# Performance work log

Measured on AMD Instinct MI355X. Metric: run time of the kernel, lower is better.

The kernel has to match this reference:

```python
import jax, jax.numpy as jnp
import numpy as np

B, LQ, LKV = 2, 2048, 2048
C, CTX, H, DK = 1024, 768, 16, 64
SCALE = DK ** (-0.5)


def setup_inputs() -> dict:
    key = jax.random.key(0)
    kx, ky, kq, kkv, kp, kb = jax.random.split(key, 6)
    # weights stored as [in, out] so projection is x @ W
    return {
        "x": jax.random.normal(kx, (B, LQ, C), dtype=jnp.float32),
        "y": jax.random.normal(ky, (B, LKV, CTX), dtype=jnp.float32),
        "Wq": jax.random.normal(kq, (C, H * DK), dtype=jnp.float32) * (C ** -0.5),
        "Wkv": jax.random.normal(kkv, (CTX, 2 * H * DK), dtype=jnp.float32) * (CTX ** -0.5),
        "Wproj": jax.random.normal(kp, (H * DK, C), dtype=jnp.float32) * ((H * DK) ** -0.5),
        "bproj": jax.random.normal(kb, (C,), dtype=jnp.float32) * 0.01,
    }


def reference(x, y, Wq, Wkv, Wproj, bproj):
    b, lq, _ = x.shape
    lkv = y.shape[1]
    # Q projection: [b, lq, H*DK] -> [b, H, lq, DK]
    q = (x @ Wq).reshape(b, lq, H, DK).transpose(0, 2, 1, 3)
    kv = (y @ Wkv).reshape(b, lkv, 2, H, DK).transpose(2, 0, 3, 1, 4)
    k, v = kv[0], kv[1]
    # attention scores [b, H, lq, lkv], stable softmax, no dropout (Identity)
    atten = jax.nn.softmax(jnp.einsum("bhid,bhjd->bhij", q, k) * SCALE, axis=-1)
    res = jnp.einsum("bhij,bhjd->bhid", atten, v)  # [b, H, lq, DK]
    res = res.transpose(0, 2, 1, 3).reshape(b, lq, H * DK)
    out = res @ Wproj + bproj  # [b, lq, C]
    return out
```

## Files before the change

kernel.cpp:

```cpp
#include <hip/hip_runtime.h>
#include <hip/hip_bf16.h>
#include <cstdint>

typedef unsigned short u16;
typedef __attribute__((ext_vector_type(4))) float f32x4;
typedef __attribute__((ext_vector_type(8))) short s16x8;
typedef __attribute__((ext_vector_type(4))) unsigned int u32x4;

#define B_    2
#define LQ_   2048
#define LKV_  2048
#define H_    16
#define QSCALE_ 0.18033688011112042f

__device__ __forceinline__ u16 f2b(float f) {
  union { float f; unsigned int u; } v; v.f = f;
  unsigned int r = v.u + 0x7fffu + ((v.u >> 16) & 1u);
  return (u16)(r >> 16);
}

__device__ __forceinline__ unsigned cvtpk(float lo, float hi) {
  unsigned r;
  asm("v_cvt_pk_bf16_f32 %0, %1, %2" : "=v"(r) : "v"(lo), "v"(hi));
  return r;
}

#if __has_builtin(__builtin_amdgcn_exp2f)
__device__ __forceinline__ float fexp2(float x) { return __builtin_amdgcn_exp2f(x); }
#else
__device__ __forceinline__ float fexp2(float x) {
  float r; asm volatile("v_exp_f32 %0, %1" : "=v"(r) : "v"(x)); return r;
}
#endif

#define GLOAD(g, l) __builtin_amdgcn_global_load_lds( \
    (const __attribute__((address_space(1))) void*)(g), \
    (__attribute__((address_space(3))) void*)(l), 16, 0, 0)

__global__ void prep(const float* __restrict__ x, u16* __restrict__ xb,
                     const float* __restrict__ y, u16* __restrict__ yb,
                     const float* __restrict__ Wq, u16* __restrict__ WqT,
                     const float* __restrict__ Wkv, u16* __restrict__ WkvT,
                     const float* __restrict__ Wp, u16* __restrict__ WpT) {
  __shared__ u16 tile[64][65];
  const int bid = blockIdx.x;
  const int t = threadIdx.x;
  if (bid < 7168) {
    const float* in; u16* out; int i;
    if (bid < 4096) { in = x; out = xb; i = (bid * 256 + t) * 4; }
    else            { in = y; out = yb; i = ((bid - 4096) * 256 + t) * 4; }
    float4 v = *reinterpret_cast<const float4*>(in + i);
    ushort4 r;
    r.x = f2b(v.x); r.y = f2b(v.y); r.z = f2b(v.z); r.w = f2b(v.w);
    *reinterpret_cast<ushort4*>(out + i) = r;
    return;
  }
  const int tb = bid - 7168;
  const float* W; u16* WT; int K, N, bx, by;
  if (tb < 256)      { W = Wq;  WT = WqT;  K = 1024; N = 1024; bx = tb & 15;         by = tb >> 4; }
  else if (tb < 640) { W = Wkv; WT = WkvT; K = 768;  N = 2048; bx = (tb - 256) & 31; by = (tb - 256) >> 5; }
  else               { W = Wp;  WT = WpT;  K = 1024; N = 1024; bx = (tb - 640) & 15; by = (tb - 640) >> 4; }
  const int n0 = bx * 64, k0 = by * 64;
#pragma unroll
  for (int p = 0; p < 4; ++p) {
    int r = (t >> 4) + p * 16;
    int c = (t & 15) * 4;
    float4 v = *reinterpret_cast<const float4*>(W + (size_t)(k0 + r) * N + n0 + c);
    tile[r][c + 0] = f2b(v.x);
    tile[r][c + 1] = f2b(v.y);
    tile[r][c + 2] = f2b(v.z);
    tile[r][c + 3] = f2b(v.w);
  }
  __syncthreads();
#pragma unroll
  for (int p = 0; p < 4; ++p) {
    int nr = (t >> 4) + p * 16;
    int kc = (t & 15) * 4;
    ushort4 o;
    o.x = tile[kc + 0][nr];
    o.y = tile[kc + 1][nr];
    o.z = tile[kc + 2][nr];
    o.w = tile[kc + 3][nr];
    *reinterpret_cast<ushort4*>(WT + (size_t)(n0 + nr) * K + k0 + kc) = o;
  }
}

__device__ __forceinline__ void gemm_core(
    int OM, const u16* __restrict__ A, const u16* __restrict__ BT,
    u16* __restrict__ Cb, float* __restrict__ Cf,
    const float* __restrict__ bias, u16* __restrict__ VTp,
    int N, int K, int m0, int n0, char* smem) {
  const int tid = threadIdx.x;
  const int w = tid >> 6, lane = tid & 63;
  const int l16 = lane & 15, lk = lane >> 4;
  const int wm = w >> 1, wn = w & 1;
  const int NS = K >> 6;

  f32x4 acc[4][2];
#pragma unroll
  for (int i = 0; i < 4; ++i)
#pragma unroll
    for (int j = 0; j < 2; ++j)
      acc[i][j] = (f32x4){0.f, 0.f, 0.f, 0.f};

  const int srow = tid >> 3;
  const int sck = (tid & 7) ^ (srow & 7);
  const u16* gA = A + (size_t)(m0 + srow) * K + sck * 8;
  const u16* gB = BT + (size_t)(n0 + srow) * K + sck * 8;
  char* dA = smem + w * 1024;
  char* dB = smem + 32768 + w * 1024;

  auto stage = [&](int k0, int bb) {
#pragma unroll
    for (int i = 0; i < 4; ++i)
      GLOAD(gA + (size_t)i * 32 * K + k0, dA + bb * 16384 + i * 4096);
#pragma unroll
    for (int i = 0; i < 2; ++i)
      GLOAD(gB + (size_t)i * 32 * K + k0, dB + bb * 8192 + i * 4096);
  };

  const int swa = (l16 & 7) << 4;

  stage(0, 0);
  __syncthreads();
  int cur = 0;
  for (int s = 0; s < NS; ++s) {
    if (s + 1 < NS) stage((s + 1) * 64, cur ^ 1);
    const char* sAb = smem + cur * 16384;
    const char* sBb = smem + 32768 + cur * 8192;
#pragma unroll
    for (int kk = 0; kk < 2; ++kk) {
      s16x8 af[4], bf[2];
#pragma unroll
      for (int mt = 0; mt < 4; ++mt)
        af[mt] = *reinterpret_cast<const s16x8*>(
            sAb + (wm * 64 + mt * 16 + l16) * 128 + ((kk * 64 + lk * 16) ^ swa));
#pragma unroll
      for (int nt = 0; nt < 2; ++nt)
        bf[nt] = *reinterpret_cast<const s16x8*>(
            sBb + (wn * 32 + nt * 16 + l16) * 128 + ((kk * 64 + lk * 16) ^ swa));
      __builtin_amdgcn_s_setprio(1);
#pragma unroll
      for (int mt = 0; mt < 4; ++mt)
#pragma unroll
        for (int nt = 0; nt < 2; ++nt)
          acc[mt][nt] = __builtin_amdgcn_mfma_f32_16x16x32_bf16(af[mt], bf[nt], acc[mt][nt], 0, 0, 0);
      __builtin_amdgcn_s_setprio(0);
    }
    __syncthreads();
    cur ^= 1;
  }

#pragma unroll
  for (int mt = 0; mt < 4; ++mt) {
#pragma unroll
    for (int nt = 0; nt < 2; ++nt) {
      const int col = n0 + wn * 32 + nt * 16 + l16;
      const int row0 = m0 + wm * 64 + mt * 16 + lk * 4;
      if (OM == 2 && col >= 1024) {
        int b = row0 >> 11, kv = row0 & 2047;
        int h = (col >> 6) & 15, d = col & 63;
        ushort4 o;
        o.x = f2b(acc[mt][nt][0]); o.y = f2b(acc[mt][nt][1]);
        o.z = f2b(acc[mt][nt][2]); o.w = f2b(acc[mt][nt][3]);
        *reinterpret_cast<ushort4*>(VTp + (((size_t)(b * 16 + h) * 64 + d) * 2048 + kv)) = o;
      } else {
#pragma unroll
        for (int j = 0; j < 4; ++j) {
          int row = row0 + j;
          if (OM == 3)      Cb[(size_t)row * N + col] = f2b(acc[mt][nt][j] * QSCALE_);
          else if (OM == 2) Cb[(size_t)row * 1024 + col] = f2b(acc[mt][nt][j]);
          else              Cf[(size_t)row * N + col] = acc[mt][nt][j] + bias[col];
        }
      }
    }
  }
}

__global__ __launch_bounds__(256, 3)
void gemm_qkv(const u16* __restrict__ xb, const u16* __restrict__ WqT,
              const u16* __restrict__ yb, const u16* __restrict__ WkvT,
              u16* __restrict__ Qb, u16* __restrict__ Kbf, u16* __restrict__ VTb) {
  __shared__ __attribute__((aligned(16))) char smem[49152];
  const int bid = blockIdx.x;
  if (bid < 512) {
    gemm_core(3, xb, WqT, Qb, nullptr, nullptr, nullptr,
              1024, 1024, (bid & 31) * 128, (bid >> 5) * 64, smem);
  } else {
    const int t = bid - 512;
    gemm_core(2, yb, WkvT, Kbf, nullptr, nullptr, VTb,
              2048, 768, (t & 31) * 128, (t >> 5) * 64, smem);
  }
}

__global__ __launch_bounds__(256, 3)
void gemm_proj(const u16* __restrict__ Rb, const u16* __restrict__ WpT,
               float* __restrict__ out, const float* __restrict__ bias) {
  __shared__ __attribute__((aligned(16))) char smem[49152];
  const int bid = blockIdx.x;
  gemm_core(1, Rb, WpT, nullptr, out, bias, nullptr,
            1024, 1024, (bid & 31) * 128, (bid >> 5) * 64, smem);
}

__global__ __launch_bounds__(512, 4)
void flash_attn(const u16* __restrict__ Kq, const u16* __restrict__ Qb,
                const u16* __restrict__ VT, u16* __restrict__ Rb) {
  __shared__ __attribute__((aligned(16))) char smem[65536];
  __shared__ float dmerge[512 * 2];

  const int tid = threadIdx.x;
  const int w = tid >> 6, l = tid & 63;
  const int l16 = l & 15, lk = l >> 4;
  const int half = w >> 2, w4 = w & 3;

  const int bid = blockIdx.x;
  const int wg = ((bid & 7) << 6) | (bid >> 3);
  const int qt = wg & 15, bh = wg >> 4;
  const int b = bh >> 4, h = bh & 15;
  const int qrow0 = qt * 128 + w4 * 32;

  const u16* qp = Qb + ((size_t)(b * LQ_ + qrow0 + l16)) * 1024 + h * 64;
  s16x8 qf[2][2];
#pragma unroll
  for (int g = 0; g < 2; ++g)
#pragma unroll
    for (int ksq = 0; ksq < 2; ++ksq)
      qf[g][ksq] = *reinterpret_cast<const s16x8*>(qp + g * 16 * 1024 + ksq * 32 + lk * 8);

  f32x4 Oacc[2][4], Osum[2];
#pragma unroll
  for (int g = 0; g < 2; ++g) {
    Osum[g] = (f32x4){0.f, 0.f, 0.f, 0.f};
#pragma unroll
    for (int dt = 0; dt < 4; ++dt) Oacc[g][dt] = (f32x4){0.f, 0.f, 0.f, 0.f};
  }

  const u16* Kg = Kq + ((size_t)(b * LKV_ + half * 1024)) * 1024 + h * 64;
  const u16* Vg = VT + ((size_t)bh * 64) * 2048 + half * 1024;
  char* Kl = smem + half * 32768;
  char* Vl = smem + half * 32768 + 16384;

  s16x8 ones;
#pragma unroll
  for (int i = 0; i < 8; ++i) ones[i] = (short)0x3F80;

  const int r0 = ((l16 >> 2) << 3) + (l16 & 3);
  const int swk = ((l16 & 3) | (((l16 >> 2) & 1) << 2)) << 4;
  const int swv = (l16 & 7) << 4;

  const int srow = (tid & 255) >> 3;
  const int sck = (tid & 7) ^ ((srow & 3) | (((srow >> 3) & 1) << 2));
  const int scv = (tid & 7) ^ (srow & 7);
  const u16* kp0 = Kg + (size_t)srow * 1024 + sck * 8;
  const u16* kp1 = kp0 + (size_t)32 * 1024;
  const u16* vp0 = Vg + (size_t)srow * 2048 + scv * 8;
  const u16* vp1 = vp0 + (size_t)32 * 2048;
  char* kd0 = Kl + w4 * 1024;
  char* vd0 = Vl + w4 * 1024;

  auto stage = [&](int bb) {
    GLOAD(kp0, kd0 + bb * 8192);
    GLOAD(kp1, kd0 + bb * 8192 + 4096);
    GLOAD(vp0, vd0 + bb * 8192);
    GLOAD(vp1, vd0 + bb * 8192 + 4096);
  };

  stage(0);
  kp0 += 65536; kp1 += 65536; vp0 += 64; vp1 += 64;
  __syncthreads();

  int cur = 0;
  for (int jt = 0; jt < 16; ++jt) {
    if (jt < 15) {
      stage(cur ^ 1);
      kp0 += 65536; kp1 += 65536; vp0 += 64; vp1 += 64;
    }
    const char* kb = Kl + cur * 8192;
    const char* vb = Vl + cur * 8192;

    f32x4 sacc[2][4];
#pragma unroll
    for (int g = 0; g < 2; ++g)
#pragma unroll
      for (int ct = 0; ct < 4; ++ct) sacc[g][ct] = (f32x4){0.f, 0.f, 0.f, 0.f};

    __builtin_amdgcn_s_setprio(1);
#pragma unroll
    for (int ct = 0; ct < 4; ++ct) {
      const int R = r0 + ((ct & 1) << 2) + ((ct >> 1) << 5);
      const char* rp = kb + R * 128;
      s16x8 ka0 = *reinterpret_cast<const s16x8*>(rp + ((lk * 16) ^ swk));
      s16x8 ka1 = *reinterpret_cast<const s16x8*>(rp + ((64 + lk * 16) ^ swk));
      sacc[0][ct] = __builtin_amdgcn_mfma_f32_16x16x32_bf16(ka0, qf[0][0], sacc[0][ct], 0, 0, 0);
      sacc[0][ct] = __builtin_amdgcn_mfma_f32_16x16x32_bf16(ka1, qf[0][1], sacc[0][ct], 0, 0, 0);
      sacc[1][ct] = __builtin_amdgcn_mfma_f32_16x16x32_bf16(ka0, qf[1][0], sacc[1][ct], 0, 0, 0);
      sacc[1][ct] = __builtin_amdgcn_mfma_f32_16x16x32_bf16(ka1, qf[1][1], sacc[1][ct], 0, 0, 0);
    }
    __builtin_amdgcn_s_setprio(0);

#pragma unroll
    for (int g = 0; g < 2; ++g)
#pragma unroll
      for (int ct = 0; ct < 4; ++ct)
#pragma unroll
        for (int j = 0; j < 4; ++j)
          sacc[g][ct][j] = fexp2(sacc[g][ct][j]);

#pragma unroll
    for (int f = 0; f < 2; ++f) {
      s16x8 va[4];
#pragma unroll
      for (int dt = 0; dt < 4; ++dt)
        va[dt] = *reinterpret_cast<const s16x8*>(vb + (dt * 16 + l16) * 128 + ((f * 64 + lk * 16) ^ swv));
      s16x8 pf[2];
#pragma unroll
      for (int g = 0; g < 2; ++g) {
        const f32x4 pA = sacc[g][2 * f];
        const f32x4 pB = sacc[g][2 * f + 1];
        union { unsigned u[4]; s16x8 v; } pk;
        pk.u[0] = cvtpk(pA[0], pA[1]);
        pk.u[1] = cvtpk(pA[2], pA[3]);
        pk.u[2] = cvtpk(pB[0], pB[1]);
        pk.u[3] = cvtpk(pB[2], pB[3]);
        pf[g] = pk.v;
      }
      __builtin_amdgcn_s_setprio(1);
#pragma unroll
      for (int dt = 0; dt < 4; ++dt) {
        Oacc[0][dt] = __builtin_amdgcn_mfma_f32_16x16x32_bf16(va[dt], pf[0], Oacc[0][dt], 0, 0, 0);
        Oacc[1][dt] = __builtin_amdgcn_mfma_f32_16x16x32_bf16(va[dt], pf[1], Oacc[1][dt], 0, 0, 0);
      }
      Osum[0] = __builtin_amdgcn_mfma_f32_16x16x32_bf16(ones, pf[0], Osum[0], 0, 0, 0);
      Osum[1] = __builtin_amdgcn_mfma_f32_16x16x32_bf16(ones, pf[1], Osum[1], 0, 0, 0);
      __builtin_amdgcn_s_setprio(0);
    }
    __syncthreads();
    cur ^= 1;
  }

  if (w >= 4) {
    char* mb = smem + (((w - 4) * 64 + l) * 128);
#pragma unroll
    for (int g = 0; g < 2; ++g)
#pragma unroll
      for (int dt = 0; dt < 4; ++dt)
        *reinterpret_cast<f32x4*>(mb + (((g * 4 + dt) * 16) ^ ((l & 7) << 4))) = Oacc[g][dt];
    dmerge[((w - 4) * 64 + l) * 2 + 0] = Osum[0][0];
    dmerge[((w - 4) * 64 + l) * 2 + 1] = Osum[1][0];
  }
  __syncthreads();
  if (w < 4) {
    const char* mb = smem + ((w * 64 + l) * 128);
#pragma unroll
    for (int g = 0; g < 2; ++g) {
      float inv = 1.f / (Osum[g][0] + dmerge[(w * 64 + l) * 2 + g]);
      u16* op = Rb + ((size_t)(b * LQ_ + qrow0 + g * 16 + l16)) * 1024 + h * 64 + lk * 4;
#pragma unroll
      for (int dt = 0; dt < 4; ++dt) {
        f32x4 o2 = *reinterpret_cast<const f32x4*>(mb + (((g * 4 + dt) * 16) ^ ((l & 7) << 4)));
        f32x4 s = Oacc[g][dt] + o2;
        ushort4 o;
        o.x = f2b(s[0] * inv); o.y = f2b(s[1] * inv);
        o.z = f2b(s[2] * inv); o.w = f2b(s[3] * inv);
        *reinterpret_cast<ushort4*>(op + dt * 16) = o;
      }
    }
  }
}

extern "C" void kernel_launch(void* const* d_in, const int* in_sizes, int n_in,
                              void* d_out, int out_size, void* d_ws, size_t ws_size,
                              hipStream_t stream) {
  const float* x   = (const float*)d_in[0];
  const float* y   = (const float*)d_in[1];
  const float* Wq  = (const float*)d_in[2];
  const float* Wkv = (const float*)d_in[3];
  const float* Wp  = (const float*)d_in[4];
  const float* bp  = (const float*)d_in[5];
  float* out = (float*)d_out;

  u16* p = (u16*)d_ws;
  u16* xb   = p; p += (size_t)4096 * 1024;
  u16* yb   = p; p += (size_t)4096 * 768;
  u16* WqT  = p; p += (size_t)1024 * 1024;
  u16* WkvT = p; p += (size_t)2048 * 768;
  u16* WpT  = p; p += (size_t)1024 * 1024;
  u16* Qb   = p; p += (size_t)4096 * 1024;
  u16* Kbf  = p; p += (size_t)4096 * 1024;
  u16* VTb  = p; p += (size_t)4096 * 1024;
  u16* Rb   = p; p += (size_t)4096 * 1024;

  prep<<<8064, 256, 0, stream>>>(x, xb, y, yb, Wq, WqT, Wkv, WkvT, Wp, WpT);

  gemm_qkv<<<1536, 256, 0, stream>>>(xb, WqT, yb, WkvT, Qb, Kbf, VTb);
  flash_attn<<<512, 512, 0, stream>>>(Kbf, Qb, VTb, Rb);
  gemm_proj<<<512, 256, 0, stream>>>(Rb, WpT, out, bp);
}
```

Before: 99.73 us.

## Rewrite QKV GEMM with 128x128 tiles and XCD-aware block remap

Replaces the QKV projection GEMM with a new templated kernel that uses 128x128 output tiles (4x4 MFMA per wave), a 32-wide K step with a single 16KB LDS buffer, and a block-index remap that spreads work across the 8 XCDs. The grid is halved to 768 blocks. Larger tiles are meant to improve operand reuse and cut global traffic. In exchange the pipeline loses double buffering and syncs twice per short K step, which may expose load latency. The old generic gemm_core is trimmed to only the projection output path.

```diff
diff --git a/kernel.cpp b/kernel.cpp
--- a/kernel.cpp
+++ b/kernel.cpp
@@ -85,6 +85,100 @@
   }
 }
 
+template <int OM>
+__device__ __forceinline__ void gemm_m97(
+    const u16* __restrict__ A, const u16* __restrict__ BT,
+    u16* __restrict__ Cb, float* __restrict__ Cf,
+    const float* __restrict__ bias, u16* __restrict__ VTp,
+    int N, int K, int m0, int n0, char* smem) {
+  const int tid = threadIdx.x;
+  const int w = tid >> 6, lane = tid & 63;
+  const int l16 = lane & 15, lk = lane >> 4;
+  const int wm = w >> 1, wn = w & 1;
+  const int NS = K >> 5;
+
+  f32x4 acc[4][4];
+#pragma unroll
+  for (int i = 0; i < 4; ++i)
+#pragma unroll
+    for (int j = 0; j < 4; ++j)
+      acc[i][j] = (f32x4){0.f, 0.f, 0.f, 0.f};
+
+  const int srow = tid & 127;
+  const u16* gA = A + (size_t)(m0 + srow) * K + (tid >> 7) * 8;
+  const u16* gB = BT + (size_t)(n0 + srow) * K + (tid >> 7) * 8;
+  char* dA = smem + w * 1024;
+  char* dB = smem + 8192 + w * 1024;
+
+  for (int s = 0; s < NS; ++s) {
+    const int k0 = s * 32;
+    GLOAD(gA + k0,      dA);
+    GLOAD(gA + k0 + 16, dA + 4096);
+    GLOAD(gB + k0,      dB);
+    GLOAD(gB + k0 + 16, dB + 4096);
+    __syncthreads();
+    s16x8 af[4], bf[4];
+    const char* pA = smem + lk * 2048;
+    const char* pB = smem + 8192 + lk * 2048;
+#pragma unroll
+    for (int mt = 0; mt < 4; ++mt)
+      af[mt] = *reinterpret_cast<const s16x8*>(pA + (wm * 64 + mt * 16 + l16) * 16);
+#pragma unroll
+    for (int nt = 0; nt < 4; ++nt)
+      bf[nt] = *reinterpret_cast<const s16x8*>(pB + (wn * 64 + nt * 16 + l16) * 16);
+    __builtin_amdgcn_s_setprio(1);
+#pragma unroll
+    for (int mt = 0; mt < 4; ++mt)
+#pragma unroll
+      for (int nt = 0; nt < 4; ++nt)
+        acc[mt][nt] = __builtin_amdgcn_mfma_f32_16x16x32_bf16(af[mt], bf[nt], acc[mt][nt], 0, 0, 0);
+    __builtin_amdgcn_s_setprio(0);
+    __syncthreads();
+  }
+
+#pragma unroll
+  for (int mt = 0; mt < 4; ++mt) {
+#pragma unroll
+    for (int nt = 0; nt < 4; ++nt) {
+      const int col = n0 + wn * 64 + nt * 16 + l16;
+      const int row0 = m0 + wm * 64 + mt * 16 + lk * 4;
+      if (OM == 2 && col >= 1024) {
+        int b = row0 >> 11, kv = row0 & 2047;
+        int h = (col >> 6) & 15, d = col & 63;
+        ushort4 o;
+        o.x = f2b(acc[mt][nt][0]); o.y = f2b(acc[mt][nt][1]);
+        o.z = f2b(acc[mt][nt][2]); o.w = f2b(acc[mt][nt][3]);
+        *reinterpret_cast<ushort4*>(VTp + (((size_t)(b * 16 + h) * 64 + d) * 2048 + kv)) = o;
+      } else {
+#pragma unroll
+        for (int j = 0; j < 4; ++j) {
+          int row = row0 + j;
+          if (OM == 3)      Cb[(size_t)row * N + col] = f2b(acc[mt][nt][j] * QSCALE_);
+          else if (OM == 2) Cb[(size_t)row * 1024 + col] = f2b(acc[mt][nt][j]);
+          else              Cf[(size_t)row * N + col] = acc[mt][nt][j] + bias[col];
+        }
+      }
+    }
+  }
+}
+
+__global__ __launch_bounds__(256, 3)
+void gemm_qkv(const u16* __restrict__ xb, const u16* __restrict__ WqT,
+              const u16* __restrict__ yb, const u16* __restrict__ WkvT,
+              u16* __restrict__ Qb, u16* __restrict__ Kbf, u16* __restrict__ VTb) {
+  __shared__ __attribute__((aligned(16))) char smem[16384];
+  const int bid = blockIdx.x;
+  const int wg = (bid & 7) * 96 + (bid >> 3);
+  if (wg < 256) {
+    gemm_m97<3>(xb, WqT, Qb, nullptr, nullptr, nullptr,
+                1024, 1024, (wg & 31) * 128, (wg >> 5) * 128, smem);
+  } else {
+    const int t = wg - 256;
+    gemm_m97<2>(yb, WkvT, Kbf, nullptr, nullptr, VTb,
+                2048, 768, (t & 31) * 128, (t >> 5) * 128, smem);
+  }
+}
+
 __device__ __forceinline__ void gemm_core(
     int OM, const u16* __restrict__ A, const u16* __restrict__ BT,
     u16* __restrict__ Cb, float* __restrict__ Cf,
@@ -157,39 +251,12 @@
     for (int nt = 0; nt < 2; ++nt) {
       const int col = n0 + wn * 32 + nt * 16 + l16;
       const int row0 = m0 + wm * 64 + mt * 16 + lk * 4;
-      if (OM == 2 && col >= 1024) {
-        int b = row0 >> 11, kv = row0 & 2047;
-        int h = (col >> 6) & 15, d = col & 63;
-        ushort4 o;
-        o.x = f2b(acc[mt][nt][0]); o.y = f2b(acc[mt][nt][1]);
-        o.z = f2b(acc[mt][nt][2]); o.w = f2b(acc[mt][nt][3]);
-        *reinterpret_cast<ushort4*>(VTp + (((size_t)(b * 16 + h) * 64 + d) * 2048 + kv)) = o;
-      } else {
-#pragma unroll
-        for (int j = 0; j < 4; ++j) {
-          int row = row0 + j;
-          if (OM == 3)      Cb[(size_t)row * N + col] = f2b(acc[mt][nt][j] * QSCALE_);
-          else if (OM == 2) Cb[(size_t)row * 1024 + col] = f2b(acc[mt][nt][j]);
-          else              Cf[(size_t)row * N + col] = acc[mt][nt][j] + bias[col];
-        }
+#pragma unroll
+      for (int j = 0; j < 4; ++j) {
+        int row = row0 + j;
+        Cf[(size_t)row * N + col] = acc[mt][nt][j] + bias[col];
       }
     }
-  }
-}
-
-__global__ __launch_bounds__(256, 3)
-void gemm_qkv(const u16* __restrict__ xb, const u16* __restrict__ WqT,
-              const u16* __restrict__ yb, const u16* __restrict__ WkvT,
-              u16* __restrict__ Qb, u16* __restrict__ Kbf, u16* __restrict__ VTb) {
-  __shared__ __attribute__((aligned(16))) char smem[49152];
-  const int bid = blockIdx.x;
-  if (bid < 512) {
-    gemm_core(3, xb, WqT, Qb, nullptr, nullptr, nullptr,
-              1024, 1024, (bid & 31) * 128, (bid >> 5) * 64, smem);
-  } else {
-    const int t = bid - 512;
-    gemm_core(2, yb, WkvT, Kbf, nullptr, nullptr, VTb,
-              2048, 768, (t & 31) * 128, (t >> 5) * 64, smem);
   }
 }
 
@@ -392,7 +459,7 @@
 
   prep<<<8064, 256, 0, stream>>>(x, xb, y, yb, Wq, WqT, Wkv, WkvT, Wp, WpT);
 
-  gemm_qkv<<<1536, 256, 0, stream>>>(xb, WqT, yb, WkvT, Qb, Kbf, VTb);
+  gemm_qkv<<<768, 256, 0, stream>>>(xb, WqT, yb, WkvT, Qb, Kbf, VTb);
   flash_attn<<<512, 512, 0, stream>>>(Kbf, Qb, VTb, Rb);
   gemm_proj<<<512, 256, 0, stream>>>(Rb, WpT, out, bp);
 }
```

Result: slower. 125.9 us (+26.3%).

## Give each attention wave 64 query rows, halving waves per block

Applied to the files above, without the earlier changes.

The flash attention kernel now runs 4 waves per block instead of 8. Each wave handles 64 query rows (4 MFMA groups) instead of 32, so every K/V fragment read from LDS feeds twice as many MFMAs. This cuts LDS read traffic per FLOP. The cost is higher register pressure from 4x4 accumulators, fewer waves to hide latency, and more global-load instructions per thread when staging.

```diff
diff --git a/kernel.cpp b/kernel.cpp
--- a/kernel.cpp
+++ b/kernel.cpp
@@ -202,34 +202,34 @@
             1024, 1024, (bid & 31) * 128, (bid >> 5) * 64, smem);
 }
 
-__global__ __launch_bounds__(512, 4)
+__global__ __launch_bounds__(256, 2)
 void flash_attn(const u16* __restrict__ Kq, const u16* __restrict__ Qb,
                 const u16* __restrict__ VT, u16* __restrict__ Rb) {
   __shared__ __attribute__((aligned(16))) char smem[65536];
-  __shared__ float dmerge[512 * 2];
+  __shared__ float dmerge[640];
 
   const int tid = threadIdx.x;
   const int w = tid >> 6, l = tid & 63;
   const int l16 = l & 15, lk = l >> 4;
-  const int half = w >> 2, w4 = w & 3;
+  const int half = w >> 1, qs = w & 1;
 
   const int bid = blockIdx.x;
   const int wg = ((bid & 7) << 6) | (bid >> 3);
   const int qt = wg & 15, bh = wg >> 4;
   const int b = bh >> 4, h = bh & 15;
-  const int qrow0 = qt * 128 + w4 * 32;
+  const int qrow0 = qt * 128 + qs * 64;
 
   const u16* qp = Qb + ((size_t)(b * LQ_ + qrow0 + l16)) * 1024 + h * 64;
-  s16x8 qf[2][2];
-#pragma unroll
-  for (int g = 0; g < 2; ++g)
+  s16x8 qf[4][2];
+#pragma unroll
+  for (int g = 0; g < 4; ++g)
 #pragma unroll
     for (int ksq = 0; ksq < 2; ++ksq)
       qf[g][ksq] = *reinterpret_cast<const s16x8*>(qp + g * 16 * 1024 + ksq * 32 + lk * 8);
 
-  f32x4 Oacc[2][4], Osum[2];
-#pragma unroll
-  for (int g = 0; g < 2; ++g) {
+  f32x4 Oacc[4][4], Osum[4];
+#pragma unroll
+  for (int g = 0; g < 4; ++g) {
     Osum[g] = (f32x4){0.f, 0.f, 0.f, 0.f};
 #pragma unroll
     for (int dt = 0; dt < 4; ++dt) Oacc[g][dt] = (f32x4){0.f, 0.f, 0.f, 0.f};
@@ -248,39 +248,40 @@
   const int swk = ((l16 & 3) | (((l16 >> 2) & 1) << 2)) << 4;
   const int swv = (l16 & 7) << 4;
 
-  const int srow = (tid & 255) >> 3;
-  const int sck = (tid & 7) ^ ((srow & 3) | (((srow >> 3) & 1) << 2));
-  const int scv = (tid & 7) ^ (srow & 7);
-  const u16* kp0 = Kg + (size_t)srow * 1024 + sck * 8;
-  const u16* kp1 = kp0 + (size_t)32 * 1024;
-  const u16* vp0 = Vg + (size_t)srow * 2048 + scv * 8;
-  const u16* vp1 = vp0 + (size_t)32 * 2048;
-  char* kd0 = Kl + w4 * 1024;
-  char* vd0 = Vl + w4 * 1024;
+  const int ht = tid & 127;
+  const int srow = ht >> 3;
+  const int c8 = ht & 7;
+  const int sck = c8 ^ ((srow & 3) | (((srow >> 3) & 1) << 2));
+  const int scv = c8 ^ (srow & 7);
+  const u16* kp = Kg + (size_t)srow * 1024 + sck * 8;
+  const u16* vp = Vg + (size_t)srow * 2048 + scv * 8;
+  char* kd = Kl + qs * 1024;
+  char* vd = Vl + qs * 1024;
 
   auto stage = [&](int bb) {
-    GLOAD(kp0, kd0 + bb * 8192);
-    GLOAD(kp1, kd0 + bb * 8192 + 4096);
-    GLOAD(vp0, vd0 + bb * 8192);
-    GLOAD(vp1, vd0 + bb * 8192 + 4096);
+#pragma unroll
+    for (int i = 0; i < 4; ++i) {
+      GLOAD(kp + (size_t)(16 * i) * 1024, kd + bb * 8192 + i * 2048);
+      GLOAD(vp + (size_t)(16 * i) * 2048, vd + bb * 8192 + i * 2048);
+    }
   };
 
   stage(0);
-  kp0 += 65536; kp1 += 65536; vp0 += 64; vp1 += 64;
+  kp += 65536; vp += 64;
   __syncthreads();
 
   int cur = 0;
   for (int jt = 0; jt < 16; ++jt) {
     if (jt < 15) {
       stage(cur ^ 1);
-      kp0 += 65536; kp1 += 65536; vp0 += 64; vp1 += 64;
+      kp += 65536; vp += 64;
     }
     const char* kb = Kl + cur * 8192;
     const char* vb = Vl + cur * 8192;
 
-    f32x4 sacc[2][4];
-#pragma unroll
-    for (int g = 0; g < 2; ++g)
+    f32x4 sacc[4][4];
+#pragma unroll
+    for (int g = 0; g < 4; ++g)
 #pragma unroll
       for (int ct = 0; ct < 4; ++ct) sacc[g][ct] = (f32x4){0.f, 0.f, 0.f, 0.f};
 
@@ -291,15 +292,16 @@
       const char* rp = kb + R * 128;
       s16x8 ka0 = *reinterpret_cast<const s16x8*>(rp + ((lk * 16) ^ swk));
       s16x8 ka1 = *reinterpret_cast<const s16x8*>(rp + ((64 + lk * 16) ^ swk));
-      sacc[0][ct] = __builtin_amdgcn_mfma_f32_16x16x32_bf16(ka0, qf[0][0], sacc[0][ct], 0, 0, 0);
-      sacc[0][ct] = __builtin_amdgcn_mfma_f32_16x16x32_bf16(ka1, qf[0][1], sacc[0][ct], 0, 0, 0);
-      sacc[1][ct] = __builtin_amdgcn_mfma_f32_16x16x32_bf16(ka0, qf[1][0], sacc[1][ct], 0, 0, 0);
-      sacc[1][ct] = __builtin_amdgcn_mfma_f32_16x16x32_bf16(ka1, qf[1][1], sacc[1][ct], 0, 0, 0);
+#pragma unroll
+      for (int g = 0; g < 4; ++g) {
+        sacc[g][ct] = __builtin_amdgcn_mfma_f32_16x16x32_bf16(ka0, qf[g][0], sacc[g][ct], 0, 0, 0);
+        sacc[g][ct] = __builtin_amdgcn_mfma_f32_16x16x32_bf16(ka1, qf[g][1], sacc[g][ct], 0, 0, 0);
+      }
     }
     __builtin_amdgcn_s_setprio(0);
 
 #pragma unroll
-    for (int g = 0; g < 2; ++g)
+    for (int g = 0; g < 4; ++g)
 #pragma unroll
       for (int ct = 0; ct < 4; ++ct)
 #pragma unroll
@@ -312,9 +314,9 @@
 #pragma unroll
       for (int dt = 0; dt < 4; ++dt)
         va[dt] = *reinterpret_cast<const s16x8*>(vb + (dt * 16 + l16) * 128 + ((f * 64 + lk * 16) ^ swv));
-      s16x8 pf[2];
-#pragma unroll
-      for (int g = 0; g < 2; ++g) {
+      s16x8 pf[4];
+#pragma unroll
+      for (int g = 0; g < 4; ++g) {
         const f32x4 pA = sacc[g][2 * f];
         const f32x4 pB = sacc[g][2 * f + 1];
         union { unsigned u[4]; s16x8 v; } pk;
@@ -326,34 +328,36 @@
       }
       __builtin_amdgcn_s_setprio(1);
 #pragma unroll
-      for (int dt = 0; dt < 4; ++dt) {
-        Oacc[0][dt] = __builtin_amdgcn_mfma_f32_16x16x32_bf16(va[dt], pf[0], Oacc[0][dt], 0, 0, 0);
-        Oacc[1][dt] = __builtin_amdgcn_mfma_f32_16x16x32_bf16(va[dt], pf[1], Oacc[1][dt], 0, 0, 0);
-      }
-      Osum[0] = __builtin_amdgcn_mfma_f32_16x16x32_bf16(ones, pf[0], Osum[0], 0, 0, 0);
-      Osum[1] = __builtin_amdgcn_mfma_f32_16x16x32_bf16(ones, pf[1], Osum[1], 0, 0, 0);
+      for (int dt = 0; dt < 4; ++dt)
+#pragma unroll
+        for (int g = 0; g < 4; ++g)
+          Oacc[g][dt] = __builtin_amdgcn_mfma_f32_16x16x32_bf16(va[dt], pf[g], Oacc[g][dt], 0, 0, 0);
+#pragma unroll
+      for (int g = 0; g < 4; ++g)
+        Osum[g] = __builtin_amdgcn_mfma_f32_16x16x32_bf16(ones, pf[g], Osum[g], 0, 0, 0);
       __builtin_amdgcn_s_setprio(0);
     }
     __syncthreads();
     cur ^= 1;
   }
 
-  if (w >= 4) {
-    char* mb = smem + (((w - 4) * 64 + l) * 128);
-#pragma unroll
-    for (int g = 0; g < 2; ++g)
+  if (half == 1) {
+    char* mb = smem + qs * 16384 + l * 256;
+#pragma unroll
+    for (int g = 0; g < 4; ++g)
 #pragma unroll
       for (int dt = 0; dt < 4; ++dt)
         *reinterpret_cast<f32x4*>(mb + (((g * 4 + dt) * 16) ^ ((l & 7) << 4))) = Oacc[g][dt];
-    dmerge[((w - 4) * 64 + l) * 2 + 0] = Osum[0][0];
-    dmerge[((w - 4) * 64 + l) * 2 + 1] = Osum[1][0];
+#pragma unroll
+    for (int g = 0; g < 4; ++g)
+      dmerge[(qs * 64 + l) * 5 + g] = Osum[g][0];
   }
   __syncthreads();
-  if (w < 4) {
-    const char* mb = smem + ((w * 64 + l) * 128);
-#pragma unroll
-    for (int g = 0; g < 2; ++g) {
-      float inv = 1.f / (Osum[g][0] + dmerge[(w * 64 + l) * 2 + g]);
+  if (half == 0) {
+    const char* mb = smem + qs * 16384 + l * 256;
+#pragma unroll
+    for (int g = 0; g < 4; ++g) {
+      float inv = 1.f / (Osum[g][0] + dmerge[(qs * 64 + l) * 5 + g]);
       u16* op = Rb + ((size_t)(b * LQ_ + qrow0 + g * 16 + l16)) * 1024 + h * 64 + lk * 4;
 #pragma unroll
       for (int dt = 0; dt < 4; ++dt) {
@@ -393,6 +397,6 @@
   prep<<<8064, 256, 0, stream>>>(x, xb, y, yb, Wq, WqT, Wkv, WkvT, Wp, WpT);
 
   gemm_qkv<<<1536, 256, 0, stream>>>(xb, WqT, yb, WkvT, Qb, Kbf, VTb);
-  flash_attn<<<512, 512, 0, stream>>>(Kbf, Qb, VTb, Rb);
+  flash_attn<<<512, 256, 0, stream>>>(Kbf, Qb, VTb, Rb);
   gemm_proj<<<512, 256, 0, stream>>>(Rb, WpT, out, bp);
 }
```

After: 99.69 us, median of 2. About the same (-0.0%).
